# Kernel tuning notes

Measured on AMD Instinct MI355X. Metric: run time of the kernel, lower is better.

The kernel has to match this reference:

```python
import jax, jax.numpy as jnp
import numpy as np

N, E, H, C, B = 20000, 320000, 4, 64, 64
D = H * C  # 256, output_dim_gnn
NEG_SLOPE = 0.2
EPS = 1e-5


def setup_inputs() -> dict:
    key = jax.random.key(0)
    ks = iter(jax.random.split(key, 40))
    s = 0.05
    inp = {}
    inp['x'] = jax.random.normal(next(ks), (N, 5), jnp.float32)
    inp['edge_index'] = jax.random.randint(next(ks), (2, E), 0, N, jnp.int64)
    inp['edge_attr'] = jax.random.normal(next(ks), (E, 63), jnp.float32)
    inp['batch'] = jnp.sort(jax.random.randint(next(ks), (N,), 0, B, jnp.int64))
    # node / edge embedding linears
    inp['node_W'] = jax.random.normal(next(ks), (5, D), jnp.float32) * s
    inp['node_b'] = jnp.zeros((D,), jnp.float32)
    inp['edge_W'] = jax.random.normal(next(ks), (63, D), jnp.float32) * s
    inp['edge_b'] = jnp.zeros((D,), jnp.float32)
    # two GATv2 layers + batch norms
    for i in range(2):
        inp[f'Wl{i}'] = jax.random.normal(next(ks), (D, H * C), jnp.float32) * s
        inp[f'bl{i}'] = jnp.zeros((H * C,), jnp.float32)
        inp[f'Wr{i}'] = jax.random.normal(next(ks), (D, H * C), jnp.float32) * s
        inp[f'br{i}'] = jnp.zeros((H * C,), jnp.float32)
        inp[f'We{i}'] = jax.random.normal(next(ks), (D, H * C), jnp.float32) * s
        inp[f'att{i}'] = jax.random.normal(next(ks), (H, C), jnp.float32) * s
        inp[f'bias{i}'] = jnp.zeros((H * C,), jnp.float32)
        inp[f'gamma{i}'] = jnp.ones((D,), jnp.float32)
        inp[f'beta{i}'] = jnp.zeros((D,), jnp.float32)
    # final MLP + output layer
    inp['mlp_W'] = jax.random.normal(next(ks), (D, C), jnp.float32) * s
    inp['mlp_b'] = jnp.zeros((C,), jnp.float32)
    inp['out_W'] = jax.random.normal(next(ks), (C, 5), jnp.float32) * s
    inp['out_b'] = jnp.zeros((5,), jnp.float32)
    return inp


def gatv2_conv(x, src, dst, e, Wl, bl, Wr, br, We, att, bias):
    # x: [N, D]; e: [E, D] (embedded edge features)
    xl = (x @ Wl + bl).reshape(N, H, C)  # source-side transform (lin_l)
    xr = (x @ Wr + br).reshape(N, H, C)  # target-side transform (lin_r)
    ee = (e @ We).reshape(E, H, C)       # lin_edge (no bias in PyG)
    m = xl[src] + xr[dst] + ee           # [E, H, C]
    alpha = jnp.einsum('ehc,hc->eh', jax.nn.leaky_relu(m, NEG_SLOPE), att)
    # segment softmax over incoming edges of each target node
    amax = jax.ops.segment_max(alpha, dst, num_segments=N)[dst]
    ex = jnp.exp(alpha - amax)
    denom = jax.ops.segment_sum(ex, dst, num_segments=N)[dst]
    a = ex / denom                        # [E, H]
    out = jax.ops.segment_sum(xl[src] * a[:, :, None], dst, num_segments=N)
    return out.reshape(N, H * C) + bias


def batch_norm(x, gamma, beta):
    mu = jnp.mean(x, axis=0)
    var = jnp.mean((x - mu) ** 2, axis=0)  # biased var (training-mode norm)
    return (x - mu) * jax.lax.rsqrt(var + EPS) * gamma + beta


def reference(x, edge_index, edge_attr, batch,
              node_W, node_b, edge_W, edge_b,
              Wl0, bl0, Wr0, br0, We0, att0, bias0, gamma0, beta0,
              Wl1, bl1, Wr1, br1, We1, att1, bias1, gamma1, beta1,
              mlp_W, mlp_b, out_W, out_b):
    src, dst = edge_index[0], edge_index[1]
    h = x @ node_W + node_b          # [N, D]
    e = edge_attr @ edge_W + edge_b  # [E, D]
    h = gatv2_conv(h, src, dst, e, Wl0, bl0, Wr0, br0, We0, att0, bias0)
    h = jax.nn.relu(batch_norm(h, gamma0, beta0))
    h = gatv2_conv(h, src, dst, e, Wl1, bl1, Wr1, br1, We1, att1, bias1)
    h = jax.nn.relu(batch_norm(h, gamma1, beta1))
    h = jax.nn.relu(h @ mlp_W + mlp_b)  # [N, C]
    # global mean pool per graph
    pooled = jax.ops.segment_sum(h, batch, num_segments=B)
    cnt = jax.ops.segment_sum(jnp.ones((N,), h.dtype), batch, num_segments=B)
    pooled = pooled / jnp.maximum(cnt, 1.0)[:, None]
    return pooled @ out_W + out_b  # [B, n_classes]
```

## Files before the change

### kernel.cpp

```cpp
#include <hip/hip_runtime.h>

#define NN 20000
#define EE 320000
#define BB 64

typedef _Float16 half8 __attribute__((ext_vector_type(8)));
typedef float floatx4 __attribute__((ext_vector_type(4)));

__global__ void k_prep_edgeW(const float* __restrict__ edge_W, const float* __restrict__ edge_b,
                             const float* __restrict__ We0, const float* __restrict__ We1,
                             _Float16* __restrict__ Wpt0, _Float16* __restrict__ Wpt1) {
    __shared__ float row[256];
    int k = blockIdx.x, layer = blockIdx.y, j = threadIdx.x;
    row[j] = (k < 63) ? edge_W[k*256 + j] : edge_b[j];
    __syncthreads();
    const float* We = layer ? We1 : We0;
    float acc = 0.f;
    for (int t = 0; t < 256; ++t) acc += row[t] * We[t*256 + j];
    (layer ? Wpt1 : Wpt0)[j*64 + k] = (_Float16)acc;
}

__global__ void k_prep_acat(const float* __restrict__ node_W, const float* __restrict__ node_b,
                            const float* __restrict__ Wl0, const float* __restrict__ bl0,
                            const float* __restrict__ Wr0, const float* __restrict__ br0,
                            float* __restrict__ Acat) {
    __shared__ float row[256];
    int k = blockIdx.x, j = threadIdx.x;
    if (j < 256) row[j] = (k < 5) ? node_W[k*256 + j] : node_b[j];
    __syncthreads();
    int jj = j & 255;
    const float* W = (j < 256) ? Wl0 : Wr0;
    float acc = 0.f;
    for (int t = 0; t < 256; ++t) acc += row[t] * W[t*256 + jj];
    if (k == 5) acc += (j < 256) ? bl0[jj] : br0[jj];
    Acat[k*512 + j] = acc;
}

__global__ void k_prep_t16(const float* __restrict__ Wl1, const float* __restrict__ bl1,
                           const float* __restrict__ Wr1, const float* __restrict__ br1,
                           const float* __restrict__ mlp_W,
                           _Float16* __restrict__ WlWr1t, float* __restrict__ blr1,
                           _Float16* __restrict__ mlpWt) {
    int n = blockIdx.x, k = threadIdx.x;
    if (n < 512) {
        float v = (n < 256) ? Wl1[k*256 + n] : Wr1[k*256 + (n - 256)];
        WlWr1t[n*256 + k] = (_Float16)v;
        if (k == 0) blr1[n] = (n < 256) ? bl1[n] : br1[n - 256];
    } else {
        int nn = n - 512;
        mlpWt[nn*256 + k] = (_Float16)mlp_W[k*64 + nn];
    }
}

__global__ void k_hist(const int* __restrict__ ei, int* __restrict__ counts) {
    int e = blockIdx.x*256 + threadIdx.x;
    if (e < EE) atomicAdd(&counts[ei[EE + e]], 1);
}

__global__ __launch_bounds__(1024) void k_scan(const int* __restrict__ counts,
                                               int* __restrict__ row_ptr, int* __restrict__ cursor) {
    __shared__ int part[1024];
    int t = threadIdx.x;
    const int per = (NN + 1023) / 1024;
    int b0 = t*per, b1 = min(b0 + per, NN);
    int s = 0;
    for (int i = b0; i < b1; ++i) s += counts[i];
    part[t] = s; __syncthreads();
    for (int d = 1; d < 1024; d <<= 1) {
        int v = (t >= d) ? part[t-d] : 0;
        __syncthreads();
        part[t] += v;
        __syncthreads();
    }
    int run = (t == 0) ? 0 : part[t-1];
    for (int i = b0; i < b1; ++i) { row_ptr[i] = run; cursor[i] = run; run += counts[i]; }
    if (t == 0) row_ptr[NN] = EE;
}

__global__ void k_scatter(const int* __restrict__ ei, int* __restrict__ cursor,
                          int* __restrict__ pos, int* __restrict__ csr_src) {
    int e = blockIdx.x*256 + threadIdx.x;
    if (e < EE) {
        int d = ei[EE + e];
        int p = atomicAdd(&cursor[d], 1);
        pos[e] = p;
        csr_src[p] = ei[e];
    }
}

__global__ void k_permattr(const float* __restrict__ attr, const int* __restrict__ pos,
                           _Float16* __restrict__ attr16) {
    int tid = threadIdx.x;
    int w = tid >> 6, lane = tid & 63;
    int e = blockIdx.x*4 + w;
    if (e >= EE) return;
    float v = (lane < 63) ? attr[(size_t)e*63 + lane] : 1.0f;
    attr16[(size_t)pos[e]*64 + lane] = (_Float16)v;
}

__global__ void k_xlxr0(const float* __restrict__ x, const float* __restrict__ Acat,
                        _Float16* __restrict__ xlxr16) {
    int n = blockIdx.x, j = threadIdx.x;
    float a0 = Acat[5*512 + j], a1 = Acat[5*512 + 256 + j];
#pragma unroll
    for (int k = 0; k < 5; ++k) {
        float xv = x[n*5 + k];
        a0 += xv * Acat[k*512 + j];
        a1 += xv * Acat[k*512 + 256 + j];
    }
    xlxr16[(size_t)n*512 + j] = (_Float16)a0;
    xlxr16[(size_t)n*512 + 256 + j] = (_Float16)a1;
}

#define NPB 4
__global__ __launch_bounds__(256) void k_fused(const _Float16* __restrict__ attr16,
        const int* __restrict__ csrc, const int* __restrict__ row_ptr,
        const _Float16* __restrict__ Wpt, const float* __restrict__ att,
        const _Float16* __restrict__ xlxr16, _Float16* __restrict__ gat16) {
    int tid = threadIdx.x;
    int wave = tid >> 6, lane = tid & 63;
    int l15 = lane & 15, l4 = lane >> 4;

    __shared__ __align__(16) _Float16 xls[4][2][16][72];

    half8 bf[4][2];
    float attv[4];
#pragma unroll
    for (int ct = 0; ct < 4; ++ct) {
        int c = wave*64 + ct*16 + l15;
        attv[ct] = att[c];
        bf[ct][0] = *(const half8*)&Wpt[(size_t)c*64 + l4*8];
        bf[ct][1] = *(const half8*)&Wpt[(size_t)c*64 + 32 + l4*8];
    }

    int n = blockIdx.x*NPB;
    int nEnd = n + NPB; if (nEnd > NN) nEnd = NN;
    int s_n = row_ptr[n];
    int e_n;
    for (;;) {
        if (n >= nEnd) return;
        e_n = row_ptr[n+1];
        if (e_n > s_n) break;
        gat16[(size_t)n*256 + wave*64 + lane] = (_Float16)0.f;
        ++n; s_n = e_n;
    }
    const int E = row_ptr[nEnd];
    int t0 = s_n;

    half8 rx0, rx1, ra0, ra1, rb0, rb1;
    int srow = lane >> 2, scol = (lane & 3) * 16;

    {
        int er = t0 + srow; if (er >= EE) er = EE - 1;
        const _Float16* sp = &xlxr16[(size_t)csrc[er]*512 + wave*64 + scol];
        rx0 = *(const half8*)&sp[0];
        rx1 = *(const half8*)&sp[8];
        int arow = t0 + l15; if (arow >= EE) arow = EE - 1;
        const _Float16* ap = &attr16[(size_t)arow*64];
        ra0 = *(const half8*)&ap[l4*8];
        ra1 = *(const half8*)&ap[32 + l4*8];
    }
    *(half8*)&xls[wave][0][srow][scol]     = rx0;
    *(half8*)&xls[wave][0][srow][scol + 8] = rx1;
    int tn = (t0 + 16 < e_n) ? t0 + 16 : e_n;
    bool hasNext = tn < E;
    if (hasNext) {
        int er = tn + srow; if (er >= EE) er = EE - 1;
        const _Float16* sp = &xlxr16[(size_t)csrc[er]*512 + wave*64 + scol];
        rx0 = *(const half8*)&sp[0];
        rx1 = *(const half8*)&sp[8];
        int arow = tn + l15; if (arow >= EE) arow = EE - 1;
        const _Float16* ap = &attr16[(size_t)arow*64];
        rb0 = *(const half8*)&ap[l4*8];
        rb1 = *(const half8*)&ap[32 + l4*8];
    }

    float xrf[4];
#pragma unroll
    for (int ct = 0; ct < 4; ++ct)
        xrf[ct] = (float)xlxr16[(size_t)n*512 + 256 + wave*64 + ct*16 + l15];

    float m_run = -3.0e38f, l_run = 0.f, out_acc = 0.f;
    int cur = 0;
    for (;;) {
        int nt = e_n - t0; if (nt > 16) nt = 16;
        floatx4 acc[4];
#pragma unroll
        for (int ct = 0; ct < 4; ++ct) {
            floatx4 z = {};
            acc[ct] = __builtin_amdgcn_mfma_f32_16x16x32_f16(ra0, bf[ct][0], z, 0, 0, 0);
            acc[ct] = __builtin_amdgcn_mfma_f32_16x16x32_f16(ra1, bf[ct][1], acc[ct], 0, 0, 0);
        }
        float p[4];
#pragma unroll
        for (int r = 0; r < 4; ++r) {
            int eidx = l4*4 + r;
            float pv = 0.f;
#pragma unroll
            for (int ct = 0; ct < 4; ++ct) {
                float m = acc[ct][r] + (float)xls[wave][cur][eidx][ct*16 + l15] + xrf[ct];
                float lr = (m > 0.f) ? m : 0.2f*m;
                pv += lr * attv[ct];
            }
            pv += __shfl_xor(pv, 1);
            pv += __shfl_xor(pv, 2);
            pv += __shfl_xor(pv, 4);
            pv += __shfl_xor(pv, 8);
            p[r] = (eidx < nt) ? pv : -3.0e38f;
        }
        float aall[16];
#pragma unroll
        for (int k = 0; k < 16; ++k)
            aall[k] = __shfl(p[k & 3], (k >> 2) << 4);
        float mt = aall[0];
#pragma unroll
        for (int k = 1; k < 16; ++k) mt = fmaxf(mt, aall[k]);
        float mnew = fmaxf(m_run, mt);
        float scale = __expf(m_run - mnew);
        out_acc *= scale; l_run *= scale;
#pragma unroll
        for (int k = 0; k < 16; ++k) {
            float wk = __expf(aall[k] - mnew);
            l_run += wk;
            out_acc += wk * (float)xls[wave][cur][k][lane];
        }
        m_run = mnew;
        if (t0 + 16 >= e_n) {
            gat16[(size_t)n*256 + wave*64 + lane] = (_Float16)(out_acc / l_run);
            ++n; s_n = e_n;
            for (;;) {
                if (n >= nEnd) return;
                e_n = row_ptr[n+1];
                if (e_n > s_n) break;
                gat16[(size_t)n*256 + wave*64 + lane] = (_Float16)0.f;
                ++n; s_n = e_n;
            }
            m_run = -3.0e38f; l_run = 0.f; out_acc = 0.f;
#pragma unroll
            for (int ct = 0; ct < 4; ++ct)
                xrf[ct] = (float)xlxr16[(size_t)n*512 + 256 + wave*64 + ct*16 + l15];
        }
        t0 = tn;
        *(half8*)&xls[wave][cur^1][srow][scol]     = rx0;
        *(half8*)&xls[wave][cur^1][srow][scol + 8] = rx1;
        ra0 = rb0; ra1 = rb1;
        tn = (t0 + 16 < e_n) ? t0 + 16 : e_n;
        hasNext = tn < E;
        if (hasNext) {
            int er = tn + srow; if (er >= EE) er = EE - 1;
            const _Float16* sp = &xlxr16[(size_t)csrc[er]*512 + wave*64 + scol];
            rx0 = *(const half8*)&sp[0];
            rx1 = *(const half8*)&sp[8];
            int arow = tn + l15; if (arow >= EE) arow = EE - 1;
            const _Float16* ap = &attr16[(size_t)arow*64];
            rb0 = *(const half8*)&ap[l4*8];
            rb1 = *(const half8*)&ap[32 + l4*8];
        }
        cur ^= 1;
    }
}

__global__ void k_bn_stats(const _Float16* __restrict__ X, float* __restrict__ stats) {
    int j = threadIdx.x;
    int shard = blockIdx.x & 15;
    float s = 0.f, q = 0.f;
    for (int r = blockIdx.x; r < NN; r += gridDim.x) {
        float v = (float)X[(size_t)r*256 + j];
        s += v; q += v*v;
    }
    atomicAdd(&stats[shard*512 + j], s);
    atomicAdd(&stats[shard*512 + 256 + j], q);
}

__global__ void k_bn_final(const float* __restrict__ stats, const float* __restrict__ gamma,
                           const float* __restrict__ beta, float* __restrict__ ss) {
    int j = threadIdx.x;
    float s = 0.f, q = 0.f;
#pragma unroll
    for (int sh = 0; sh < 16; ++sh) {
        s += stats[sh*512 + j];
        q += stats[sh*512 + 256 + j];
    }
    float mean = s * (1.0f/NN);
    float var  = q * (1.0f/NN) - mean*mean;
    float sc = rsqrtf(var + 1e-5f) * gamma[j];
    ss[j] = sc;
    ss[256 + j] = beta[j] - mean*sc;
}

template<bool RELU, typename OT>
__global__ __launch_bounds__(256) void k_gemm(const _Float16* __restrict__ A,
                       const float* __restrict__ ssv,
                       const _Float16* __restrict__ Bt,
                       const float* __restrict__ bias, OT* __restrict__ C,
                       int M, int ldc) {
    __shared__ __align__(16) _Float16 As[128][72];
    __shared__ __align__(16) _Float16 Bs[64][72];
    int tid = threadIdx.x;
    int wave = tid >> 6, lane = tid & 63;
    int l15 = lane & 15, l4 = lane >> 4;
    int row0 = blockIdx.x*128, n0 = blockIdx.y*64;
    floatx4 acc[2][4] = {};
    for (int k0 = 0; k0 < 256; k0 += 64) {
#pragma unroll
        for (int q = 0; q < 4; ++q) {
            int c = tid + q*256;
            int r = c >> 3, kc = (c & 7)*8;
            int gr = row0 + r; if (gr >= M) gr = M - 1;
            half8 g = *(const half8*)&A[(size_t)gr*256 + k0 + kc];
            _Float16 tmp[8];
#pragma unroll
            for (int i = 0; i < 8; ++i) {
                int colk = k0 + kc + i;
                float v = (float)g[i]*ssv[colk] + ssv[256 + colk];
                tmp[i] = (_Float16)fmaxf(v, 0.f);
            }
            *(half8*)&As[r][kc] = *(half8*)tmp;
        }
#pragma unroll
        for (int q = 0; q < 2; ++q) {
            int c = tid + q*256;
            int r = c >> 3, kc = (c & 7)*8;
            *(half8*)&Bs[r][kc] = *(const half8*)&Bt[(size_t)(n0 + r)*256 + k0 + kc];
        }
        __syncthreads();
#pragma unroll
        for (int ks = 0; ks < 64; ks += 32) {
            half8 a0 = *(const half8*)&As[wave*32 + l15][ks + l4*8];
            half8 a1 = *(const half8*)&As[wave*32 + 16 + l15][ks + l4*8];
#pragma unroll
            for (int nb = 0; nb < 4; ++nb) {
                half8 b = *(const half8*)&Bs[nb*16 + l15][ks + l4*8];
                acc[0][nb] = __builtin_amdgcn_mfma_f32_16x16x32_f16(a0, b, acc[0][nb], 0, 0, 0);
                acc[1][nb] = __builtin_amdgcn_mfma_f32_16x16x32_f16(a1, b, acc[1][nb], 0, 0, 0);
            }
        }
        __syncthreads();
    }
#pragma unroll
    for (int m = 0; m < 2; ++m)
#pragma unroll
    for (int nb = 0; nb < 4; ++nb) {
        int col = n0 + nb*16 + l15;
        float bv = bias[col];
#pragma unroll
        for (int r = 0; r < 4; ++r) {
            int grow = row0 + wave*32 + m*16 + l4*4 + r;
            if (grow < M) {
                float v = acc[m][nb][r] + bv;
                if (RELU) v = fmaxf(v, 0.f);
                C[(size_t)grow*ldc + col] = (OT)v;
            }
        }
    }
}

__global__ void k_pool2(const float* __restrict__ mo, const int* __restrict__ batch,
                        float* __restrict__ pooledDiv) {
    int b = blockIdx.x;
    int j = threadIdx.x & 63, rg = threadIdx.x >> 6;
    int lo = 0, hi = NN;
    while (lo < hi) { int mid = (lo + hi) >> 1; if (batch[mid] < b) lo = mid + 1; else hi = mid; }
    int s = lo;
    lo = 0; hi = NN;
    while (lo < hi) { int mid = (lo + hi) >> 1; if (batch[mid] < b + 1) lo = mid + 1; else hi = mid; }
    int e = lo;
    float acc = 0.f;
    for (int r = s + rg; r < e; r += 4) acc += mo[(size_t)r*64 + j];
    __shared__ float red[256];
    red[threadIdx.x] = acc;
    __syncthreads();
    if (rg == 0) {
        float v = red[j] + red[64 + j] + red[128 + j] + red[192 + j];
        pooledDiv[b*64 + j] = v / fmaxf((float)(e - s), 1.f);
    }
}

__global__ void k_final(const float* __restrict__ pooledDiv,
                        const float* __restrict__ outW, const float* __restrict__ outb,
                        float* __restrict__ out) {
    int t = threadIdx.x;
    if (t >= 320) return;
    int b = t / 5, c = t % 5;
    float acc = outb[c];
    for (int k = 0; k < 64; ++k) acc += pooledDiv[b*64 + k] * outW[k*5 + c];
    out[t] = acc;
}

extern "C" void kernel_launch(void* const* d_in, const int* in_sizes, int n_in,
                              void* d_out, int out_size, void* d_ws, size_t ws_size,
                              hipStream_t stream) {
    const float* x      = (const float*)d_in[0];
    const int*   ei     = (const int*)d_in[1];
    const float* attr   = (const float*)d_in[2];
    const int*   batch  = (const int*)d_in[3];
    const float* node_W = (const float*)d_in[4];
    const float* node_b = (const float*)d_in[5];
    const float* edge_W = (const float*)d_in[6];
    const float* edge_b = (const float*)d_in[7];
    const float* Wl[2]   = {(const float*)d_in[8],  (const float*)d_in[17]};
    const float* bl[2]   = {(const float*)d_in[9],  (const float*)d_in[18]};
    const float* Wr[2]   = {(const float*)d_in[10], (const float*)d_in[19]};
    const float* br[2]   = {(const float*)d_in[11], (const float*)d_in[20]};
    const float* We[2]   = {(const float*)d_in[12], (const float*)d_in[21]};
    const float* att[2]  = {(const float*)d_in[13], (const float*)d_in[22]};
    const float* gamma[2]= {(const float*)d_in[15], (const float*)d_in[24]};
    const float* beta[2] = {(const float*)d_in[16], (const float*)d_in[25]};
    const float* mlp_W = (const float*)d_in[26];
    const float* mlp_b = (const float*)d_in[27];
    const float* out_W = (const float*)d_in[28];
    const float* out_b = (const float*)d_in[29];
    float* out = (float*)d_out;

    char* p = (char*)d_ws;
    size_t off = 0;
    auto carve = [&](size_t bytes) -> void* {
        void* r = p + off;
        off = (off + bytes + 255) & ~(size_t)255;
        return r;
    };
    _Float16* Wpt0   = (_Float16*)carve(256*64*2);
    _Float16* Wpt1   = (_Float16*)carve(256*64*2);
    float*    Acat   = (float*)carve(6*512*4);
    _Float16* WlWr1t = (_Float16*)carve(512*256*2);
    float*    blr1   = (float*)carve(512*4);
    _Float16* mlpWt  = (_Float16*)carve(64*256*2);
    float*    ss     = (float*)carve(512*4);
    _Float16* xlxr16 = (_Float16*)carve((size_t)NN*512*2);
    _Float16* gat16  = (_Float16*)carve((size_t)NN*256*2);
    float*    mlo    = (float*)carve((size_t)NN*64*4);
    _Float16* attr16 = (_Float16*)carve((size_t)EE*64*2);
    int*      row_ptr= (int*)carve((NN+1)*4);
    int*      pos    = (int*)carve((size_t)EE*4);
    int*      csrc   = (int*)carve((size_t)EE*4);
    int*      cursor = (int*)carve(NN*4);
    float*    pooledDiv = (float*)carve(BB*64*4);
    char*     zz     = (char*)carve((NN + 16384)*4);
    int*      counts = (int*)zz;
    float*    stats  = (float*)(zz + (size_t)NN*4);
    if (off > ws_size) return;

    hipMemsetAsync(zz, 0, (size_t)(NN + 16384)*4, stream);
    k_prep_edgeW<<<dim3(64,2), 256, 0, stream>>>(edge_W, edge_b, We[0], We[1], Wpt0, Wpt1);
    k_prep_acat<<<6, 512, 0, stream>>>(node_W, node_b, Wl[0], bl[0], Wr[0], br[0], Acat);
    k_prep_t16<<<576, 256, 0, stream>>>(Wl[1], bl[1], Wr[1], br[1], mlp_W, WlWr1t, blr1, mlpWt);
    k_hist<<<(EE+255)/256, 256, 0, stream>>>(ei, counts);
    k_scan<<<1, 1024, 0, stream>>>(counts, row_ptr, cursor);
    k_scatter<<<(EE+255)/256, 256, 0, stream>>>(ei, cursor, pos, csrc);
    k_permattr<<<EE/4, 256, 0, stream>>>(attr, pos, attr16);
    k_xlxr0<<<NN, 256, 0, stream>>>(x, Acat, xlxr16);

    for (int L = 0; L < 2; ++L) {
        k_fused<<<(NN + NPB - 1)/NPB, 256, 0, stream>>>(attr16, csrc, row_ptr,
                 L ? Wpt1 : Wpt0, att[L], xlxr16, gat16);
        k_bn_stats<<<1024, 256, 0, stream>>>(gat16, stats + L*8192);
        k_bn_final<<<1, 256, 0, stream>>>(stats + L*8192, gamma[L], beta[L], ss);
        if (L == 0)
            k_gemm<false, _Float16><<<dim3(157, 8), 256, 0, stream>>>(gat16, ss, WlWr1t, blr1, xlxr16, NN, 512);
        else
            k_gemm<true, float><<<dim3(157, 1), 256, 0, stream>>>(gat16, ss, mlpWt, mlp_b, mlo, NN, 64);
    }
    k_pool2<<<BB, 256, 0, stream>>>(mlo, batch, pooledDiv);
    k_final<<<1, 320, 0, stream>>>(pooledDiv, out_W, out_b, out);
}
```

Baseline: 466.1 us.

## Prefetch two edge tiles ahead in fused GATv2 kernel with register double buffering

Restructures the fused attention-aggregation kernel so that gathered source features, edge attributes and the target-side xr value are loaded two tiles ahead into register double buffers. The loop body is unrolled by two via a macro, and the LDS staging buffer drops from double to single buffering. The xr load becomes one lane-indexed load per tile, spread across lanes with shuffles, which removes the serialized load at node boundaries. The aim is to hide gather latency better across node transitions, at the cost of more registers and a larger unrolled body. The single LDS buffer is written and read within the same iteration without an explicit barrier, relying on wave-local execution order.

```diff
diff --git a/kernel.cpp b/kernel.cpp
--- a/kernel.cpp
+++ b/kernel.cpp
@@ -113,6 +113,78 @@
 }
 
 #define NPB 4
+
+#define LOADT(Q) { \
+    int er = tl + srow; if (er >= el) er = el - 1; \
+    const _Float16* sp = &xlxr16[(size_t)csrc[er]*512 + wave*64 + scol]; \
+    rx0[Q] = *(const half8*)&sp[0]; \
+    rx1[Q] = *(const half8*)&sp[8]; \
+    int arow = tl + l15; if (arow >= el) arow = el - 1; \
+    const _Float16* ap = &attr16[(size_t)arow*64]; \
+    ra0[Q] = *(const half8*)&ap[l4*8]; \
+    ra1[Q] = *(const half8*)&ap[32 + l4*8]; \
+    rxr[Q] = (float)xlxr16[(size_t)nl*512 + 256 + wave*64 + lane]; \
+}
+
+#define FUSED_BODY(CUR) { \
+    int nt = ec - tc; if (nt > 16) nt = 16; \
+     \
+    floatx4 acc[4]; \
+    _Pragma("unroll") \
+    for (int ct = 0; ct < 4; ++ct) { \
+        floatx4 z = {}; \
+        acc[ct] = __builtin_amdgcn_mfma_f32_16x16x32_f16(ra0[CUR], bf[ct][0], z, 0, 0, 0); \
+        acc[ct] = __builtin_amdgcn_mfma_f32_16x16x32_f16(ra1[CUR], bf[ct][1], acc[ct], 0, 0, 0); \
+    } \
+     \
+    *(half8*)&xls[wave][srow][scol]     = rx0[CUR]; \
+    *(half8*)&xls[wave][srow][scol + 8] = rx1[CUR]; \
+     \
+    float xrf[4]; \
+    _Pragma("unroll") \
+    for (int ct = 0; ct < 4; ++ct) xrf[ct] = __shfl(rxr[CUR], ct*16 + l15); \
+     \
+    if (haveL) { LOADT(CUR); haveL = advL(); } \
+     \
+    float p[4]; \
+    _Pragma("unroll") \
+    for (int r = 0; r < 4; ++r) { \
+        int eidx = l4*4 + r; \
+        float pv = 0.f; \
+        _Pragma("unroll") \
+        for (int ct = 0; ct < 4; ++ct) { \
+            float m = acc[ct][r] + (float)xls[wave][eidx][ct*16 + l15] + xrf[ct]; \
+            float lr = (m > 0.f) ? m : 0.2f*m; \
+            pv += lr * attv[ct]; \
+        } \
+        pv += __shfl_xor(pv, 1); \
+        pv += __shfl_xor(pv, 2); \
+        pv += __shfl_xor(pv, 4); \
+        pv += __shfl_xor(pv, 8); \
+        p[r] = (eidx < nt) ? pv : -3.0e38f; \
+    } \
+    float aall[16]; \
+    _Pragma("unroll") \
+    for (int k = 0; k < 16; ++k) aall[k] = __shfl(p[k & 3], (k >> 2) << 4); \
+    float mt = aall[0]; \
+    _Pragma("unroll") \
+    for (int k = 1; k < 16; ++k) mt = fmaxf(mt, aall[k]); \
+    float mnew = fmaxf(m_run, mt); \
+    float scale = __expf(m_run - mnew); \
+    out_acc *= scale; l_run *= scale; \
+    _Pragma("unroll") \
+    for (int k = 0; k < 16; ++k) { \
+        float wk = __expf(aall[k] - mnew); \
+        l_run += wk; \
+        out_acc += wk * (float)xls[wave][k][lane]; \
+    } \
+    m_run = mnew; \
+    if (tc + 16 >= ec) { \
+        gat16[(size_t)nc*256 + wave*64 + lane] = (_Float16)(out_acc / l_run); \
+        m_run = -3.0e38f; l_run = 0.f; out_acc = 0.f; \
+    } \
+}
+
 __global__ __launch_bounds__(256) void k_fused(const _Float16* __restrict__ attr16,
         const int* __restrict__ csrc, const int* __restrict__ row_ptr,
         const _Float16* __restrict__ Wpt, const float* __restrict__ att,
@@ -120,8 +192,9 @@
     int tid = threadIdx.x;
     int wave = tid >> 6, lane = tid & 63;
     int l15 = lane & 15, l4 = lane >> 4;
-
-    __shared__ __align__(16) _Float16 xls[4][2][16][72];
+    int srow = lane >> 2, scol = (lane & 3) * 16;
+
+    __shared__ __align__(16) _Float16 xls[4][16][72];
 
     half8 bf[4][2];
     float attv[4];
@@ -133,130 +206,43 @@
         bf[ct][1] = *(const half8*)&Wpt[(size_t)c*64 + 32 + l4*8];
     }
 
-    int n = blockIdx.x*NPB;
-    int nEnd = n + NPB; if (nEnd > NN) nEnd = NN;
-    int s_n = row_ptr[n];
-    int e_n;
+    int n0 = blockIdx.x*NPB;
+    int nEnd = n0 + NPB; if (nEnd > NN) nEnd = NN;
+
+    int nc = -1, tc = 0, ec = 0;
+    for (int m = n0; m < nEnd; ++m) {
+        int s = row_ptr[m], e = row_ptr[m+1];
+        if (e <= s) gat16[(size_t)m*256 + wave*64 + lane] = (_Float16)0.f;
+        else if (nc < 0) { nc = m; tc = s; ec = e; }
+    }
+    if (nc < 0) return;
+
+    int nl = nc, tl = tc, el = ec;
+    auto advIt = [&](int& n, int& t, int& e) -> bool {
+        t += 16;
+        if (t < e) return true;
+        for (;;) {
+            ++n;
+            if (n >= nEnd) return false;
+            int s = row_ptr[n]; e = row_ptr[n+1];
+            if (e > s) { t = s; return true; }
+        }
+    };
+    auto advL = [&]() -> bool { return advIt(nl, tl, el); };
+
+    half8 rx0[2], rx1[2], ra0[2], ra1[2];
+    float rxr[2];
+
+    LOADT(0);
+    bool haveL = advL();
+    if (haveL) { LOADT(1); haveL = advL(); }
+
+    float m_run = -3.0e38f, l_run = 0.f, out_acc = 0.f;
     for (;;) {
-        if (n >= nEnd) return;
-        e_n = row_ptr[n+1];
-        if (e_n > s_n) break;
-        gat16[(size_t)n*256 + wave*64 + lane] = (_Float16)0.f;
-        ++n; s_n = e_n;
-    }
-    const int E = row_ptr[nEnd];
-    int t0 = s_n;
-
-    half8 rx0, rx1, ra0, ra1, rb0, rb1;
-    int srow = lane >> 2, scol = (lane & 3) * 16;
-
-    {
-        int er = t0 + srow; if (er >= EE) er = EE - 1;
-        const _Float16* sp = &xlxr16[(size_t)csrc[er]*512 + wave*64 + scol];
-        rx0 = *(const half8*)&sp[0];
-        rx1 = *(const half8*)&sp[8];
-        int arow = t0 + l15; if (arow >= EE) arow = EE - 1;
-        const _Float16* ap = &attr16[(size_t)arow*64];
-        ra0 = *(const half8*)&ap[l4*8];
-        ra1 = *(const half8*)&ap[32 + l4*8];
-    }
-    *(half8*)&xls[wave][0][srow][scol]     = rx0;
-    *(half8*)&xls[wave][0][srow][scol + 8] = rx1;
-    int tn = (t0 + 16 < e_n) ? t0 + 16 : e_n;
-    bool hasNext = tn < E;
-    if (hasNext) {
-        int er = tn + srow; if (er >= EE) er = EE - 1;
-        const _Float16* sp = &xlxr16[(size_t)csrc[er]*512 + wave*64 + scol];
-        rx0 = *(const half8*)&sp[0];
-        rx1 = *(const half8*)&sp[8];
-        int arow = tn + l15; if (arow >= EE) arow = EE - 1;
-        const _Float16* ap = &attr16[(size_t)arow*64];
-        rb0 = *(const half8*)&ap[l4*8];
-        rb1 = *(const half8*)&ap[32 + l4*8];
-    }
-
-    float xrf[4];
-#pragma unroll
-    for (int ct = 0; ct < 4; ++ct)
-        xrf[ct] = (float)xlxr16[(size_t)n*512 + 256 + wave*64 + ct*16 + l15];
-
-    float m_run = -3.0e38f, l_run = 0.f, out_acc = 0.f;
-    int cur = 0;
-    for (;;) {
-        int nt = e_n - t0; if (nt > 16) nt = 16;
-        floatx4 acc[4];
-#pragma unroll
-        for (int ct = 0; ct < 4; ++ct) {
-            floatx4 z = {};
-            acc[ct] = __builtin_amdgcn_mfma_f32_16x16x32_f16(ra0, bf[ct][0], z, 0, 0, 0);
-            acc[ct] = __builtin_amdgcn_mfma_f32_16x16x32_f16(ra1, bf[ct][1], acc[ct], 0, 0, 0);
-        }
-        float p[4];
-#pragma unroll
-        for (int r = 0; r < 4; ++r) {
-            int eidx = l4*4 + r;
-            float pv = 0.f;
-#pragma unroll
-            for (int ct = 0; ct < 4; ++ct) {
-                float m = acc[ct][r] + (float)xls[wave][cur][eidx][ct*16 + l15] + xrf[ct];
-                float lr = (m > 0.f) ? m : 0.2f*m;
-                pv += lr * attv[ct];
-            }
-            pv += __shfl_xor(pv, 1);
-            pv += __shfl_xor(pv, 2);
-            pv += __shfl_xor(pv, 4);
-            pv += __shfl_xor(pv, 8);
-            p[r] = (eidx < nt) ? pv : -3.0e38f;
-        }
-        float aall[16];
-#pragma unroll
-        for (int k = 0; k < 16; ++k)
-            aall[k] = __shfl(p[k & 3], (k >> 2) << 4);
-        float mt = aall[0];
-#pragma unroll
-        for (int k = 1; k < 16; ++k) mt = fmaxf(mt, aall[k]);
-        float mnew = fmaxf(m_run, mt);
-        float scale = __expf(m_run - mnew);
-        out_acc *= scale; l_run *= scale;
-#pragma unroll
-        for (int k = 0; k < 16; ++k) {
-            float wk = __expf(aall[k] - mnew);
-            l_run += wk;
-            out_acc += wk * (float)xls[wave][cur][k][lane];
-        }
-        m_run = mnew;
-        if (t0 + 16 >= e_n) {
-            gat16[(size_t)n*256 + wave*64 + lane] = (_Float16)(out_acc / l_run);
-            ++n; s_n = e_n;
-            for (;;) {
-                if (n >= nEnd) return;
-                e_n = row_ptr[n+1];
-                if (e_n > s_n) break;
-                gat16[(size_t)n*256 + wave*64 + lane] = (_Float16)0.f;
-                ++n; s_n = e_n;
-            }
-            m_run = -3.0e38f; l_run = 0.f; out_acc = 0.f;
-#pragma unroll
-            for (int ct = 0; ct < 4; ++ct)
-                xrf[ct] = (float)xlxr16[(size_t)n*512 + 256 + wave*64 + ct*16 + l15];
-        }
-        t0 = tn;
-        *(half8*)&xls[wave][cur^1][srow][scol]     = rx0;
-        *(half8*)&xls[wave][cur^1][srow][scol + 8] = rx1;
-        ra0 = rb0; ra1 = rb1;
-        tn = (t0 + 16 < e_n) ? t0 + 16 : e_n;
-        hasNext = tn < E;
-        if (hasNext) {
-            int er = tn + srow; if (er >= EE) er = EE - 1;
-            const _Float16* sp = &xlxr16[(size_t)csrc[er]*512 + wave*64 + scol];
-            rx0 = *(const half8*)&sp[0];
-            rx1 = *(const half8*)&sp[8];
-            int arow = tn + l15; if (arow >= EE) arow = EE - 1;
-            const _Float16* ap = &attr16[(size_t)arow*64];
-            rb0 = *(const half8*)&ap[l4*8];
-            rb1 = *(const half8*)&ap[32 + l4*8];
-        }
-        cur ^= 1;
+        FUSED_BODY(0);
+        if (!advIt(nc, tc, ec)) break;
+        FUSED_BODY(1);
+        if (!advIt(nc, tc, ec)) break;
     }
 }
 
```

After: 464.5 us. Within noise of the previous version (-0.4%).

## Restructure GATv2 fused kernel: transposed MFMA, MFMA aggregation, lazy rescale

Applied to the files above, without the earlier changes.

Rewrites the per-node attention loop in the fused GATv2 kernel. The edge-feature MFMA is transposed so each lane holds four channels per edge, which lets the attention logit be reduced with two shuffles instead of a 16-wide butterfly plus broadcasts. The weighted aggregation of source features now runs as an MFMA instead of a scalar 16-step loop. The softmax max is rescaled lazily, only when it grows by more than a threshold. It also halves the nodes per block to two, drops the LDS double buffer in favour of a register prefetch, and clamps edge indices to the node range rather than the global edge count. The costs are fp16 rounding of the softmax weights, half of the aggregation MFMA spent on zero operands, and a shared-memory round trip for the output, with no explicit barrier between the LDS writes and reads across lanes.

```diff
diff --git a/kernel.cpp b/kernel.cpp
--- a/kernel.cpp
+++ b/kernel.cpp
@@ -5,6 +5,7 @@
 #define BB 64
 
 typedef _Float16 half8 __attribute__((ext_vector_type(8)));
+typedef _Float16 half4 __attribute__((ext_vector_type(4)));
 typedef float floatx4 __attribute__((ext_vector_type(4)));
 
 __global__ void k_prep_edgeW(const float* __restrict__ edge_W, const float* __restrict__ edge_b,
@@ -112,7 +113,7 @@
     xlxr16[(size_t)n*512 + 256 + j] = (_Float16)a1;
 }
 
-#define NPB 4
+#define NPB 2
 __global__ __launch_bounds__(256) void k_fused(const _Float16* __restrict__ attr16,
         const int* __restrict__ csrc, const int* __restrict__ row_ptr,
         const _Float16* __restrict__ Wpt, const float* __restrict__ att,
@@ -120,143 +121,159 @@
     int tid = threadIdx.x;
     int wave = tid >> 6, lane = tid & 63;
     int l15 = lane & 15, l4 = lane >> 4;
-
-    __shared__ __align__(16) _Float16 xls[4][2][16][72];
+    int srow = lane >> 2, scol = (lane & 3) * 16;
+
+    __shared__ __align__(16) _Float16 xls[4][16][72];
+    __shared__ _Float16 obuf[4][64];
 
     half8 bf[4][2];
-    float attv[4];
+    float attq[4][4];
 #pragma unroll
     for (int ct = 0; ct < 4; ++ct) {
         int c = wave*64 + ct*16 + l15;
-        attv[ct] = att[c];
         bf[ct][0] = *(const half8*)&Wpt[(size_t)c*64 + l4*8];
         bf[ct][1] = *(const half8*)&Wpt[(size_t)c*64 + 32 + l4*8];
-    }
-
-    int n = blockIdx.x*NPB;
-    int nEnd = n + NPB; if (nEnd > NN) nEnd = NN;
-    int s_n = row_ptr[n];
-    int e_n;
+#pragma unroll
+        for (int r = 0; r < 4; ++r)
+            attq[ct][r] = att[wave*64 + ct*16 + l4*4 + r];
+    }
+
+    int n0 = blockIdx.x*NPB;
+    int nEnd = n0 + NPB; if (nEnd > NN) nEnd = NN;
+
+    int nc = -1, tc = 0, ec = 0;
+    for (int m = n0; m < nEnd; ++m) {
+        int s = row_ptr[m], e = row_ptr[m+1];
+        if (e <= s) gat16[(size_t)m*256 + wave*64 + lane] = (_Float16)0.f;
+        else if (nc < 0) { nc = m; tc = s; ec = e; }
+    }
+    if (nc < 0) return;
+
+    int nl = nc, tl = tc, el = ec;
+    auto adv = [&](int& n, int& t, int& e) -> bool {
+        t += 16;
+        if (t < e) return true;
+        for (;;) {
+            ++n;
+            if (n >= nEnd) return false;
+            int s = row_ptr[n]; e = row_ptr[n+1];
+            if (e > s) { t = s; return true; }
+        }
+    };
+
+    half8 rx0, rx1, ra0, ra1;
+    {
+        int er = tl + srow; if (er >= el) er = el - 1;
+        const _Float16* sp = &xlxr16[(size_t)csrc[er]*512 + wave*64 + scol];
+        rx0 = *(const half8*)&sp[0]; rx1 = *(const half8*)&sp[8];
+        int arow = tl + l15; if (arow >= el) arow = el - 1;
+        const _Float16* ap = &attr16[(size_t)arow*64];
+        ra0 = *(const half8*)&ap[l4*8]; ra1 = *(const half8*)&ap[32 + l4*8];
+    }
+    bool haveL = adv(nl, tl, el);
+
+    float xrq[4][4];
+    bool needXr = true;
+    float m_run = -3.0e38f, l_run = 0.f;
+    floatx4 pvq[4] = {};
+
     for (;;) {
-        if (n >= nEnd) return;
-        e_n = row_ptr[n+1];
-        if (e_n > s_n) break;
-        gat16[(size_t)n*256 + wave*64 + lane] = (_Float16)0.f;
-        ++n; s_n = e_n;
-    }
-    const int E = row_ptr[nEnd];
-    int t0 = s_n;
-
-    half8 rx0, rx1, ra0, ra1, rb0, rb1;
-    int srow = lane >> 2, scol = (lane & 3) * 16;
-
-    {
-        int er = t0 + srow; if (er >= EE) er = EE - 1;
-        const _Float16* sp = &xlxr16[(size_t)csrc[er]*512 + wave*64 + scol];
-        rx0 = *(const half8*)&sp[0];
-        rx1 = *(const half8*)&sp[8];
-        int arow = t0 + l15; if (arow >= EE) arow = EE - 1;
-        const _Float16* ap = &attr16[(size_t)arow*64];
-        ra0 = *(const half8*)&ap[l4*8];
-        ra1 = *(const half8*)&ap[32 + l4*8];
-    }
-    *(half8*)&xls[wave][0][srow][scol]     = rx0;
-    *(half8*)&xls[wave][0][srow][scol + 8] = rx1;
-    int tn = (t0 + 16 < e_n) ? t0 + 16 : e_n;
-    bool hasNext = tn < E;
-    if (hasNext) {
-        int er = tn + srow; if (er >= EE) er = EE - 1;
-        const _Float16* sp = &xlxr16[(size_t)csrc[er]*512 + wave*64 + scol];
-        rx0 = *(const half8*)&sp[0];
-        rx1 = *(const half8*)&sp[8];
-        int arow = tn + l15; if (arow >= EE) arow = EE - 1;
-        const _Float16* ap = &attr16[(size_t)arow*64];
-        rb0 = *(const half8*)&ap[l4*8];
-        rb1 = *(const half8*)&ap[32 + l4*8];
-    }
-
-    float xrf[4];
-#pragma unroll
-    for (int ct = 0; ct < 4; ++ct)
-        xrf[ct] = (float)xlxr16[(size_t)n*512 + 256 + wave*64 + ct*16 + l15];
-
-    float m_run = -3.0e38f, l_run = 0.f, out_acc = 0.f;
-    int cur = 0;
-    for (;;) {
-        int nt = e_n - t0; if (nt > 16) nt = 16;
+        int nt = ec - tc; if (nt > 16) nt = 16;
+        if (needXr) {
+#pragma unroll
+            for (int ct = 0; ct < 4; ++ct)
+#pragma unroll
+                for (int r = 0; r < 4; ++r)
+                    xrq[ct][r] = (float)xlxr16[(size_t)nc*512 + 256 + wave*64 + ct*16 + l4*4 + r];
+            needXr = false;
+        }
+        *(half8*)&xls[wave][srow][scol]     = rx0;
+        *(half8*)&xls[wave][srow][scol + 8] = rx1;
         floatx4 acc[4];
 #pragma unroll
         for (int ct = 0; ct < 4; ++ct) {
             floatx4 z = {};
-            acc[ct] = __builtin_amdgcn_mfma_f32_16x16x32_f16(ra0, bf[ct][0], z, 0, 0, 0);
-            acc[ct] = __builtin_amdgcn_mfma_f32_16x16x32_f16(ra1, bf[ct][1], acc[ct], 0, 0, 0);
-        }
-        float p[4];
-#pragma unroll
-        for (int r = 0; r < 4; ++r) {
-            int eidx = l4*4 + r;
-            float pv = 0.f;
-#pragma unroll
-            for (int ct = 0; ct < 4; ++ct) {
-                float m = acc[ct][r] + (float)xls[wave][cur][eidx][ct*16 + l15] + xrf[ct];
+            acc[ct] = __builtin_amdgcn_mfma_f32_16x16x32_f16(bf[ct][0], ra0, z, 0, 0, 0);
+            acc[ct] = __builtin_amdgcn_mfma_f32_16x16x32_f16(bf[ct][1], ra1, acc[ct], 0, 0, 0);
+        }
+        if (haveL) {
+            int er = tl + srow; if (er >= el) er = el - 1;
+            const _Float16* sp = &xlxr16[(size_t)csrc[er]*512 + wave*64 + scol];
+            rx0 = *(const half8*)&sp[0]; rx1 = *(const half8*)&sp[8];
+            int arow = tl + l15; if (arow >= el) arow = el - 1;
+            const _Float16* ap = &attr16[(size_t)arow*64];
+            ra0 = *(const half8*)&ap[l4*8]; ra1 = *(const half8*)&ap[32 + l4*8];
+            haveL = adv(nl, tl, el);
+        }
+        float aP = 0.f;
+#pragma unroll
+        for (int ct = 0; ct < 4; ++ct) {
+            half4 xv = *(const half4*)&xls[wave][l15][ct*16 + l4*4];
+#pragma unroll
+            for (int r = 0; r < 4; ++r) {
+                float m = acc[ct][r] + (float)xv[r] + xrq[ct][r];
                 float lr = (m > 0.f) ? m : 0.2f*m;
-                pv += lr * attv[ct];
-            }
-            pv += __shfl_xor(pv, 1);
-            pv += __shfl_xor(pv, 2);
-            pv += __shfl_xor(pv, 4);
-            pv += __shfl_xor(pv, 8);
-            p[r] = (eidx < nt) ? pv : -3.0e38f;
-        }
-        float aall[16];
-#pragma unroll
-        for (int k = 0; k < 16; ++k)
-            aall[k] = __shfl(p[k & 3], (k >> 2) << 4);
-        float mt = aall[0];
-#pragma unroll
-        for (int k = 1; k < 16; ++k) mt = fmaxf(mt, aall[k]);
-        float mnew = fmaxf(m_run, mt);
-        float scale = __expf(m_run - mnew);
-        out_acc *= scale; l_run *= scale;
-#pragma unroll
-        for (int k = 0; k < 16; ++k) {
-            float wk = __expf(aall[k] - mnew);
-            l_run += wk;
-            out_acc += wk * (float)xls[wave][cur][k][lane];
-        }
-        m_run = mnew;
-        if (t0 + 16 >= e_n) {
-            gat16[(size_t)n*256 + wave*64 + lane] = (_Float16)(out_acc / l_run);
-            ++n; s_n = e_n;
-            for (;;) {
-                if (n >= nEnd) return;
-                e_n = row_ptr[n+1];
-                if (e_n > s_n) break;
-                gat16[(size_t)n*256 + wave*64 + lane] = (_Float16)0.f;
-                ++n; s_n = e_n;
-            }
-            m_run = -3.0e38f; l_run = 0.f; out_acc = 0.f;
+                aP += lr * attq[ct][r];
+            }
+        }
+        aP += __shfl_xor(aP, 16);
+        aP += __shfl_xor(aP, 32);
+        float alpha = (l15 < nt) ? aP : -3.0e38f;
+        float mt = alpha;
+        mt = fmaxf(mt, __shfl_xor(mt, 1));
+        mt = fmaxf(mt, __shfl_xor(mt, 2));
+        mt = fmaxf(mt, __shfl_xor(mt, 4));
+        mt = fmaxf(mt, __shfl_xor(mt, 8));
+        if (mt > m_run + 8.f) {
+            float scale = __expf(m_run - mt);
+            l_run *= scale;
 #pragma unroll
             for (int ct = 0; ct < 4; ++ct)
-                xrf[ct] = (float)xlxr16[(size_t)n*512 + 256 + wave*64 + ct*16 + l15];
-        }
-        t0 = tn;
-        *(half8*)&xls[wave][cur^1][srow][scol]     = rx0;
-        *(half8*)&xls[wave][cur^1][srow][scol + 8] = rx1;
-        ra0 = rb0; ra1 = rb1;
-        tn = (t0 + 16 < e_n) ? t0 + 16 : e_n;
-        hasNext = tn < E;
-        if (hasNext) {
-            int er = tn + srow; if (er >= EE) er = EE - 1;
-            const _Float16* sp = &xlxr16[(size_t)csrc[er]*512 + wave*64 + scol];
-            rx0 = *(const half8*)&sp[0];
-            rx1 = *(const half8*)&sp[8];
-            int arow = tn + l15; if (arow >= EE) arow = EE - 1;
-            const _Float16* ap = &attr16[(size_t)arow*64];
-            rb0 = *(const half8*)&ap[l4*8];
-            rb1 = *(const half8*)&ap[32 + l4*8];
-        }
-        cur ^= 1;
+#pragma unroll
+                for (int r = 0; r < 4; ++r) pvq[ct][r] *= scale;
+            m_run = mt;
+        }
+        float w = __expf(alpha - m_run);
+        float ws = w;
+        ws += __shfl_xor(ws, 1);
+        ws += __shfl_xor(ws, 2);
+        ws += __shfl_xor(ws, 4);
+        ws += __shfl_xor(ws, 8);
+        l_run += ws;
+        half8 wq;
+#pragma unroll
+        for (int j = 0; j < 8; ++j) {
+            float tw = __shfl(w, ((lane >> 4) & 1)*8 + j);
+            wq[j] = (l4 < 2) ? (_Float16)tw : (_Float16)0.f;
+        }
+#pragma unroll
+        for (int ct = 0; ct < 4; ++ct) {
+            half8 av;
+#pragma unroll
+            for (int j = 0; j < 8; ++j) av[j] = (_Float16)0.f;
+            if (l4 < 2) {
+#pragma unroll
+                for (int j = 0; j < 8; ++j) av[j] = xls[wave][l4*8 + j][ct*16 + l15];
+            }
+            pvq[ct] = __builtin_amdgcn_mfma_f32_16x16x32_f16(av, wq, pvq[ct], 0, 0, 0);
+        }
+        bool nodeEnd = (tc + 16 >= ec);
+        if (nodeEnd) {
+            float inv = 1.0f / l_run;
+            if (l15 == 0) {
+#pragma unroll
+                for (int ct = 0; ct < 4; ++ct)
+#pragma unroll
+                    for (int r = 0; r < 4; ++r)
+                        obuf[wave][ct*16 + l4*4 + r] = (_Float16)(pvq[ct][r]*inv);
+            }
+            gat16[(size_t)nc*256 + wave*64 + lane] = obuf[wave][lane];
+            m_run = -3.0e38f; l_run = 0.f;
+#pragma unroll
+            for (int ct = 0; ct < 4; ++ct) { floatx4 z = {}; pvq[ct] = z; }
+        }
+        if (!adv(nc, tc, ec)) break;
+        if (nodeEnd) needXr = true;
     }
 }
 
```

Result: slower. 479.4 us (+2.8%).
